# Optimization experiments

Hardware: AMD Instinct MI355X
Metric: run time of the kernel (lower is better)

Reference implementation:

```python
import jax, jax.numpy as jnp
import numpy as np

BASE_TEMP, MIN_TEMP, MAX_TEMP = 0.07, 0.04, 0.2
B, D = 4096, 768


def setup_inputs() -> dict:
    key = jax.random.key(0)
    k1, k2, k3 = jax.random.split(key, 3)
    return {
        "vision_features": jax.random.normal(k1, (B, D), dtype=jnp.float32),
        "text_features": jax.random.normal(k2, (B, D), dtype=jnp.float32),
        "match_ids": jax.random.randint(k3, (B,), 0, 1024, dtype=jnp.int64),
    }


def reference(vision_features, text_features, match_ids):
    # L2-normalize features along the feature dim
    v = vision_features / jnp.linalg.norm(vision_features, axis=1, keepdims=True)
    t = text_features / jnp.linalg.norm(text_features, axis=1, keepdims=True)
    sim = v @ t.T  # [B, B]

    n = match_ids.shape[0]
    match = match_ids[:, None] == match_ids[None, :]  # [B, B] bool, diag True
    mf = match.astype(sim.dtype)
    eye = jnp.eye(n, dtype=sim.dtype)
    pos_mask = mf * (1.0 - eye)          # diagonal zeroed
    neg_mask = 1.0 - mf                   # diagonal also zero (was match)

    pos_mean = (pos_mask * sim).sum() / jnp.maximum(1.0, pos_mask.sum())
    neg_mean = (neg_mask * sim).sum() / jnp.maximum(1.0, neg_mask.sum())
    separation = pos_mean - neg_mean
    temp = jnp.clip(BASE_TEMP * (0.8 + 0.4 * jnp.exp(-2.0 * separation)),
                    MIN_TEMP, MAX_TEMP)

    logits = sim / temp
    # v2t: for each row i, sum over positives j of (-logits[i,j] + lse(row i))
    lse_rows = jax.nn.logsumexp(logits, axis=1)  # [B]
    v2t = (mf * (lse_rows[:, None] - logits)).sum()
    # t2v: for each column i, sum over positives j of (-logits[j,i] + lse(col i))
    lse_cols = jax.nn.logsumexp(logits, axis=0)  # [B]
    t2v = (mf * (lse_cols[None, :] - logits)).sum()

    num_pos = mf.sum()  # includes diagonal, matching the torch code
    v2t = v2t / num_pos
    t2v = t2v / num_pos
    loss = (v2t + t2v) / 2.0
    return loss
```

## Files before the change

### kernel.cpp

```cpp
#include <hip/hip_runtime.h>
#include <hip/hip_bf16.h>

#define NB 4096
#define DD 768
#define NKT 12
#define NBLK 256

typedef float f32x4 __attribute__((ext_vector_type(4)));
typedef long i64x2 __attribute__((ext_vector_type(2)));
typedef unsigned int uint;

#define WAITVM(N) asm volatile("s_waitcnt vmcnt(" #N ")" ::: "memory")

__global__ void init_kernel(float* scal, uint* bars)
{
    if (threadIdx.x < 16) scal[threadIdx.x] = 0.0f;
    bars[threadIdx.x] = 0u;
}

__device__ __forceinline__ void grid_bar(uint* bars, uint phase, int rawb, int t)
{
    __syncthreads();
    if (t == 0) {
        int g = rawb & 15;
        uint prev = __hip_atomic_fetch_add(&bars[g * 16], 1u, __ATOMIC_ACQ_REL, __HIP_MEMORY_SCOPE_AGENT);
        if (prev == phase * 16u - 1u) {
            uint r = __hip_atomic_fetch_add(&bars[384], 1u, __ATOMIC_ACQ_REL, __HIP_MEMORY_SCOPE_AGENT);
            if (r == phase * 16u - 1u)
                __hip_atomic_store(&bars[448], phase, __ATOMIC_RELEASE, __HIP_MEMORY_SCOPE_AGENT);
        }
        while (__hip_atomic_load(&bars[448], __ATOMIC_RELAXED, __HIP_MEMORY_SCOPE_AGENT) < phase)
            __builtin_amdgcn_s_sleep(8);
        (void)__hip_atomic_load(&bars[448], __ATOMIC_ACQUIRE, __HIP_MEMORY_SCOPE_AGENT);
    }
    __syncthreads();
}

__device__ __forceinline__ void stage_range(
    unsigned char* ldsAll,
    const unsigned char* __restrict__ vhat8, const unsigned char* __restrict__ that8,
    int rowBase, int colBase, int T, int i0, int i1, int wid, int lane)
{
    int u = T & 3;
    const unsigned char* src = (wid >= 4) ? that8 : vhat8;
    int tb = (wid >= 4) ? colBase : rowBase;
    int w4 = wid & 3;
    int logc = (lane & 3) ^ ((lane >> 3) & 3);
    int rowIn = w4 * 64 + (lane >> 2);
    unsigned char* dbase = ldsAll + u * 32768 + ((wid >= 4) ? 16384 : 0) + w4 * 4096;
    #pragma unroll
    for (int i = i0; i <= i1; ++i) {
        const unsigned char* g = src + (size_t)(tb + rowIn + i * 16) * DD + T * 64 + logc * 16;
        __builtin_amdgcn_global_load_lds(
            (const __attribute__((address_space(1))) void*)g,
            (__attribute__((address_space(3))) void*)(dbase + i * 1024),
            16, 0, 0);
    }
}

__global__ __launch_bounds__(512, 2) void fused_kernel(
    const float* __restrict__ vf, const float* __restrict__ tf, const int* __restrict__ ids,
    unsigned char* __restrict__ vhat8, unsigned char* __restrict__ that8,
    float* scal, float* rs, float* cs, float* cntf, int* npart, uint* bars,
    float* __restrict__ out)
{
    __shared__ unsigned char ldsAll[4 * 32768];
    __shared__ int idr[256], idc[256];
    __shared__ float red[24];
    __shared__ float rs_l[256], cs_l[256];
    __shared__ int bp[16], wred_i[8];
    __shared__ float ra[8], rn[8];
    __shared__ float invT_sh, mf_sh;

    int rawb = blockIdx.x;
    int t = threadIdx.x, wid = t >> 6, lane = t & 63;

    {
        f32x4 xr[4][3];
        uint* dsts[4];
        #pragma unroll
        for (int it = 0; it < 4; ++it) {
            int row = rawb * 32 + wid * 4 + it;
            const float* src;
            if (row < NB) { src = vf + (size_t)row * DD; dsts[it] = (uint*)(vhat8 + (size_t)row * DD); }
            else          { src = tf + (size_t)(row - NB) * DD; dsts[it] = (uint*)(that8 + (size_t)(row - NB) * DD); }
            xr[it][0] = __builtin_nontemporal_load((const f32x4*)(src + lane * 4));
            xr[it][1] = __builtin_nontemporal_load((const f32x4*)(src + 256 + lane * 4));
            xr[it][2] = __builtin_nontemporal_load((const f32x4*)(src + 512 + lane * 4));
        }
        int idreg[8];
        #pragma unroll
        for (int i = 0; i < 8; ++i) idreg[i] = ids[t + i * 512];

        #pragma unroll
        for (int it = 0; it < 4; ++it) {
            float s = 0.f;
            #pragma unroll
            for (int c = 0; c < 3; ++c)
                s += xr[it][c][0]*xr[it][c][0] + xr[it][c][1]*xr[it][c][1]
                   + xr[it][c][2]*xr[it][c][2] + xr[it][c][3]*xr[it][c][3];
            #pragma unroll
            for (int off = 1; off < 64; off <<= 1) s += __shfl_xor(s, off, 64);
            float scale = 1.0f / sqrtf(s);
            #pragma unroll
            for (int c = 0; c < 3; ++c) {
                int p = __builtin_amdgcn_cvt_pk_fp8_f32(xr[it][c][0] * scale, xr[it][c][1] * scale, 0, false);
                p = __builtin_amdgcn_cvt_pk_fp8_f32(xr[it][c][2] * scale, xr[it][c][3] * scale, p, true);
                dsts[it][c * 64 + lane] = (uint)p;
            }
        }
        int* idsh = (int*)ldsAll;
        #pragma unroll
        for (int i = 0; i < 8; ++i) idsh[t + i * 512] = idreg[i];
    }
    __syncthreads();

    {
        int* idsh = (int*)ldsAll;
        int sub = t >> 5, l32 = t & 31;
        int my = idsh[rawb * 16 + sub];
        const int4* idsh4 = (const int4*)idsh;
        int c = 0;
        #pragma unroll 8
        for (int j = l32; j < NB / 4; j += 32) {
            int4 v = idsh4[j];
            c += (v.x == my) + (v.y == my) + (v.z == my) + (v.w == my);
        }
        #pragma unroll
        for (int off = 16; off > 0; off >>= 1) c += __shfl_down(c, off, 32);
        if (l32 == 0) { cntf[rawb * 16 + sub] = (float)c; bp[sub] = c; }
    }
    if (t < 32) rs[rawb * 32 + t] = 0.0f;
    __syncthreads();
    if (t == 0) {
        int s = 0;
        #pragma unroll
        for (int i = 0; i < 16; ++i) s += bp[i];
        npart[rawb] = s;
    }

    grid_bar(bars, 1u, rawb, t);

    int rg = rawb & 7, sq = rawb >> 3;
    int by = (rg >> 1) * 4 + (sq >> 3);
    int bx = (rg & 1) * 8 + (sq & 7);
    int rowBase = by * 256, colBase = bx * 256;
    int wr = wid >> 2, wc = wid & 3;
    int fr = lane & 15, g = lane >> 4;

    f32x4 acc[8][4];
    #pragma unroll
    for (int m = 0; m < 8; ++m)
        #pragma unroll
        for (int n = 0; n < 4; ++n) acc[m][n] = (f32x4){0.f, 0.f, 0.f, 0.f};

    int pcoff = (g ^ ((fr >> 1) & 3)) * 16;
    int aoffB = (wr * 128 + fr) * 64 + pcoff;
    int boffB = 16384 + (wc * 64 + fr) * 64 + pcoff;

    stage_range(ldsAll, vhat8, that8, rowBase, colBase, 0, 0, 3, wid, lane);
    stage_range(ldsAll, vhat8, that8, rowBase, colBase, 1, 0, 3, wid, lane);
    stage_range(ldsAll, vhat8, that8, rowBase, colBase, 2, 0, 3, wid, lane);
    WAITVM(8);
    __builtin_amdgcn_s_barrier();

    for (int T = 0; T < NKT; ++T) {
        const unsigned char* U = ldsAll + (T & 3) * 32768;
        i64x2 a0[4], bb[4];
        #pragma unroll
        for (int m = 0; m < 4; ++m) a0[m] = *(const i64x2*)(U + aoffB + m * 1024);
        #pragma unroll
        for (int n = 0; n < 4; ++n) bb[n] = *(const i64x2*)(U + boffB + n * 1024);
        if (T + 3 < NKT)
            stage_range(ldsAll, vhat8, that8, rowBase, colBase, T + 3, 0, 1, wid, lane);
        __builtin_amdgcn_s_barrier();
        __builtin_amdgcn_s_setprio(1);
        #pragma unroll
        for (int m = 0; m < 4; ++m)
            #pragma unroll
            for (int n = 0; n < 4; ++n) {
                acc[m][n] = __builtin_amdgcn_mfma_f32_16x16x32_fp8_fp8(a0[m][0], bb[n][0], acc[m][n], 0, 0, 0);
                acc[m][n] = __builtin_amdgcn_mfma_f32_16x16x32_fp8_fp8(a0[m][1], bb[n][1], acc[m][n], 0, 0, 0);
            }
        __builtin_amdgcn_s_setprio(0);
        __builtin_amdgcn_s_barrier();
        i64x2 a1[4];
        #pragma unroll
        for (int m = 0; m < 4; ++m) a1[m] = *(const i64x2*)(U + aoffB + (m + 4) * 1024);
        if (T + 3 < NKT)
            stage_range(ldsAll, vhat8, that8, rowBase, colBase, T + 3, 2, 3, wid, lane);
        __builtin_amdgcn_s_barrier();
        __builtin_amdgcn_s_setprio(1);
        #pragma unroll
        for (int m = 0; m < 4; ++m)
            #pragma unroll
            for (int n = 0; n < 4; ++n) {
                acc[m + 4][n] = __builtin_amdgcn_mfma_f32_16x16x32_fp8_fp8(a1[m][0], bb[n][0], acc[m + 4][n], 0, 0, 0);
                acc[m + 4][n] = __builtin_amdgcn_mfma_f32_16x16x32_fp8_fp8(a1[m][1], bb[n][1], acc[m + 4][n], 0, 0, 0);
            }
        __builtin_amdgcn_s_setprio(0);
        if (T < NKT - 3)       { WAITVM(8); }
        else if (T == NKT - 3) { WAITVM(4); }
        else if (T == NKT - 2) { WAITVM(0); }
        __builtin_amdgcn_s_barrier();
    }

    if (t < 256) idr[t] = ids[rowBase + t];
    else         idc[t - 256] = ids[colBase + (t - 256)];
    __syncthreads();
    {
        float tsum = 0.f, msum = 0.f, dsum = 0.f;
        #pragma unroll
        for (int m = 0; m < 8; ++m) {
            int rl = wr * 128 + m * 16 + g * 4;
            #pragma unroll
            for (int n = 0; n < 4; ++n) {
                int cl = wc * 64 + n * 16 + fr;
                int colId = idc[cl];
                int gj = colBase + cl;
                #pragma unroll
                for (int r = 0; r < 4; ++r) {
                    float val = acc[m][n][r];
                    tsum += val;
                    if (idr[rl + r] == colId) msum += val;
                    if (rowBase + rl + r == gj) dsum += val;
                }
            }
        }
        #pragma unroll
        for (int off = 32; off > 0; off >>= 1) {
            tsum += __shfl_down(tsum, off, 64);
            msum += __shfl_down(msum, off, 64);
            dsum += __shfl_down(dsum, off, 64);
        }
        if (lane == 0) { red[wid] = tsum; red[8 + wid] = msum; red[16 + wid] = dsum; }
        __syncthreads();
        if (t == 0) {
            float s0 = 0.f, s1 = 0.f, s2 = 0.f;
            #pragma unroll
            for (int w = 0; w < 8; ++w) { s0 += red[w]; s1 += red[8 + w]; s2 += red[16 + w]; }
            atomicAdd(&scal[0], s0);
            atomicAdd(&scal[1], s1);
            atomicAdd(&scal[2], s2);
        }
    }

    {
        int myn = (t < NBLK) ? npart[t] : 0;
        #pragma unroll
        for (int off = 32; off > 0; off >>= 1) myn += __shfl_down(myn, off, 64);
        if (lane == 0) wred_i[wid] = myn;
    }
    if (t < 256) { rs_l[t] = 0.0f; cs_l[t] = 0.0f; }

    grid_bar(bars, 2u, rawb, t);

    if (t == 0) {
        int npi = 0;
        #pragma unroll
        for (int w = 0; w < 8; ++w) npi += wred_i[w];
        float total = __hip_atomic_load(&scal[0], __ATOMIC_RELAXED, __HIP_MEMORY_SCOPE_AGENT);
        float mf    = __hip_atomic_load(&scal[1], __ATOMIC_RELAXED, __HIP_MEMORY_SCOPE_AGENT);
        float trace = __hip_atomic_load(&scal[2], __ATOMIC_RELAXED, __HIP_MEMORY_SCOPE_AGENT);
        float np = (float)npi;
        float pos_cnt = np - (float)NB;
        float neg_cnt = (float)NB * (float)NB - np;
        float pos_mean = (mf - trace) / fmaxf(1.0f, pos_cnt);
        float neg_mean = (total - mf) / fmaxf(1.0f, neg_cnt);
        float sep = pos_mean - neg_mean;
        float temp = 0.07f * (0.8f + 0.4f * expf(-2.0f * sep));
        temp = fminf(fmaxf(temp, 0.04f), 0.2f);
        invT_sh = 1.0f / temp;
        mf_sh = mf;
    }
    __syncthreads();
    float invT = invT_sh;

    #pragma unroll
    for (int m = 0; m < 8; ++m)
        #pragma unroll
        for (int n = 0; n < 4; ++n)
            #pragma unroll
            for (int r = 0; r < 4; ++r)
                acc[m][n][r] = __expf((acc[m][n][r] - 1.0f) * invT);
    #pragma unroll
    for (int m = 0; m < 8; ++m) {
        #pragma unroll
        for (int r = 0; r < 4; ++r) {
            float rp = 0.f;
            #pragma unroll
            for (int n = 0; n < 4; ++n) rp += acc[m][n][r];
            rp += __shfl_xor(rp, 1, 64);
            rp += __shfl_xor(rp, 2, 64);
            rp += __shfl_xor(rp, 4, 64);
            rp += __shfl_xor(rp, 8, 64);
            if (fr == 0) atomicAdd(&rs_l[wr * 128 + m * 16 + g * 4 + r], rp);
        }
    }
    #pragma unroll
    for (int n = 0; n < 4; ++n) {
        float cp = 0.f;
        #pragma unroll
        for (int m = 0; m < 8; ++m)
            #pragma unroll
            for (int r = 0; r < 4; ++r) cp += acc[m][n][r];
        cp += __shfl_xor(cp, 16, 64);
        cp += __shfl_xor(cp, 32, 64);
        if (g == 0) atomicAdd(&cs_l[wc * 64 + n * 16 + fr], cp);
    }
    __syncthreads();
    if (t < 256) {
        atomicAdd(&rs[rowBase + t], rs_l[t]);
        atomicAdd(&cs[colBase + t], cs_l[t]);
    }

    grid_bar(bars, 3u, rawb, t);
    if (rawb != 0) return;

    {
        float a = 0.f, npl = 0.f;
        for (int i = t; i < NB; i += 512) {
            float cf = cntf[i];
            a += cf * (logf(rs[i]) + logf(cs[i]));
            npl += cf;
        }
        #pragma unroll
        for (int off = 32; off > 0; off >>= 1) {
            a += __shfl_down(a, off, 64);
            npl += __shfl_down(npl, off, 64);
        }
        if (lane == 0) { ra[wid] = a; rn[wid] = npl; }
        __syncthreads();
        if (t == 0) {
            float A = 0.f, np = 0.f;
            #pragma unroll
            for (int w = 0; w < 8; ++w) { A += ra[w]; np += rn[w]; }
            out[0] = (A + 2.0f * invT_sh * (np - mf_sh)) / (2.0f * np);
        }
    }
}

extern "C" void kernel_launch(void* const* d_in, const int* in_sizes, int n_in,
                              void* d_out, int out_size, void* d_ws, size_t ws_size,
                              hipStream_t stream)
{
    const float* vf  = (const float*)d_in[0];
    const float* tf  = (const float*)d_in[1];
    const int*   ids = (const int*)d_in[2];

    float* ws_f = (float*)d_ws;
    float* scal = ws_f;
    float* rs   = ws_f + 16;
    float* cs   = ws_f + 16 + 4096;
    float* cntf = ws_f + 16 + 8192;
    int* npart  = (int*)(ws_f + 16 + 12288);
    uint* bars  = (uint*)(ws_f + 16 + 12800);
    unsigned char* vhat8 = (unsigned char*)d_ws + 131072;
    unsigned char* that8 = vhat8 + (size_t)NB * DD;

    init_kernel<<<1, 512, 0, stream>>>(scal, bars);
    fused_kernel<<<NBLK, 512, 0, stream>>>(vf, tf, ids, vhat8, that8,
                                           scal, rs, cs, cntf, npart, bars, (float*)d_out);
}
```

Before: 78.40 us.

## Replace grid barriers with per-tile readiness flags and last-block ticket

Drops the first full grid barrier after the normalize/quantize phase. Each block now waits only on counters for the 8 blocks that produced its row panel and its column panel before starting the GEMM. The final grid barrier becomes a last-arriving-block ticket, so only that block does the final reduction and the other blocks exit without waiting. This is meant to cut barrier stalls, at the cost of extra flag memory and more careful memory-ordering reasoning.

```diff
diff --git a/kernel.cpp b/kernel.cpp
--- a/kernel.cpp
+++ b/kernel.cpp
@@ -14,8 +14,10 @@
 
 __global__ void init_kernel(float* scal, uint* bars)
 {
-    if (threadIdx.x < 16) scal[threadIdx.x] = 0.0f;
-    bars[threadIdx.x] = 0u;
+    int t = threadIdx.x;
+    if (t < 16) scal[t] = 0.0f;
+    bars[t] = 0u;
+    bars[512 + t] = 0u;
 }
 
 __device__ __forceinline__ void grid_bar(uint* bars, uint phase, int rawb, int t)
@@ -71,6 +73,7 @@
     __shared__ int bp[16], wred_i[8];
     __shared__ float ra[8], rn[8];
     __shared__ float invT_sh, mf_sh;
+    __shared__ uint tick_sh;
 
     int rawb = blockIdx.x;
     int t = threadIdx.x, wid = t >> 6, lane = t & 63;
@@ -114,6 +117,8 @@
         for (int i = 0; i < 8; ++i) idsh[t + i * 512] = idreg[i];
     }
     __syncthreads();
+    if (t == 0)
+        __hip_atomic_fetch_add(&bars[512 + (rawb >> 3) * 16], 1u, __ATOMIC_ACQ_REL, __HIP_MEMORY_SCOPE_AGENT);
 
     {
         int* idsh = (int*)ldsAll;
@@ -139,14 +144,25 @@
         npart[rawb] = s;
     }
 
-    grid_bar(bars, 1u, rawb, t);
-
     int rg = rawb & 7, sq = rawb >> 3;
     int by = (rg >> 1) * 4 + (sq >> 3);
     int bx = (rg & 1) * 8 + (sq & 7);
     int rowBase = by * 256, colBase = bx * 256;
     int wr = wid >> 2, wc = wid & 3;
     int fr = lane & 15, g = lane >> 4;
+
+    __syncthreads();
+    if (t == 0) {
+        uint* fA = &bars[512 + by * 16];
+        uint* fB = &bars[512 + (16 + bx) * 16];
+        while (__hip_atomic_load(fA, __ATOMIC_RELAXED, __HIP_MEMORY_SCOPE_AGENT) < 8u)
+            __builtin_amdgcn_s_sleep(4);
+        while (__hip_atomic_load(fB, __ATOMIC_RELAXED, __HIP_MEMORY_SCOPE_AGENT) < 8u)
+            __builtin_amdgcn_s_sleep(4);
+        (void)__hip_atomic_load(fA, __ATOMIC_ACQUIRE, __HIP_MEMORY_SCOPE_AGENT);
+        (void)__hip_atomic_load(fB, __ATOMIC_ACQUIRE, __HIP_MEMORY_SCOPE_AGENT);
+    }
+    __syncthreads();
 
     f32x4 acc[8][4];
     #pragma unroll
@@ -253,7 +269,7 @@
     }
     if (t < 256) { rs_l[t] = 0.0f; cs_l[t] = 0.0f; }
 
-    grid_bar(bars, 2u, rawb, t);
+    grid_bar(bars, 1u, rawb, t);
 
     if (t == 0) {
         int npi = 0;
@@ -314,8 +330,13 @@
         atomicAdd(&cs[colBase + t], cs_l[t]);
     }
 
-    grid_bar(bars, 3u, rawb, t);
-    if (rawb != 0) return;
+    __syncthreads();
+    if (t == 0) {
+        uint prev = __hip_atomic_fetch_add(&bars[464], 1u, __ATOMIC_ACQ_REL, __HIP_MEMORY_SCOPE_AGENT);
+        tick_sh = prev;
+    }
+    __syncthreads();
+    if (tick_sh != NBLK - 1) return;
 
     {
         float a = 0.f, npl = 0.f;
```

Result: no change. 77.44 us (-1.2%).
